# Optimization experiments

Measured on AMD Instinct MI355X. Metric: run time of the kernel, lower is better.

The kernel has to match this reference:

```python
import jax, jax.numpy as jnp
import numpy as np

B, A, T, D, H, NB, OUT = 64, 128, 6, 256, 512, 5, 401
ALPHA = 0.5
BETA = 0.5


def _lin_init(key, n_in, n_out, extra=()):
    bound = 1.0 / np.sqrt(n_in)
    kw, kb = jax.random.split(key)
    W = jax.random.uniform(kw, extra + (n_in, n_out), minval=-bound, maxval=bound, dtype=jnp.float32)
    b = jax.random.uniform(kb, extra + (n_out,), minval=-bound, maxval=bound, dtype=jnp.float32)
    return W, b


def setup_inputs() -> dict:
    key = jax.random.key(0)
    ks = jax.random.split(key, 8)
    stdv = 1.0 / np.sqrt(D)
    anchor = jax.random.uniform(ks[0], (1, 1, T, D), minval=-stdv, maxval=stdv, dtype=jnp.float32)
    sW1, sb1 = _lin_init(ks[1], D, D, (NB,))
    sW2, sb2 = _lin_init(ks[2], D, D, (NB,))
    cW1, cb1 = _lin_init(ks[3], D, D, (NB,))
    cW2, cb2 = _lin_init(ks[4], D, D, (NB,))
    dW1, db1 = _lin_init(ks[5], D, H)
    dW2, db2 = _lin_init(ks[6], H, OUT)
    final_embedding = jax.random.normal(ks[7], (B, A, D), dtype=jnp.float32)
    return {"final_embedding": final_embedding, "anchor": anchor,
            "sW1": sW1, "sb1": sb1, "sW2": sW2, "sb2": sb2,
            "cW1": cW1, "cb1": cb1, "cW2": cW2, "cb2": cb2,
            "dW1": dW1, "db1": db1, "dW2": dW2, "db2": db2}


def _mlp2(x, W1, b1, W2, b2):
    # 2-layer MLP (Linear -> ReLU -> Linear), applied to last dim
    return jax.nn.relu(x @ W1 + b1) @ W2 + b2


def reference(final_embedding, anchor, sW1, sb1, sW2, sb2, cW1, cb1, cW2, cb2, dW1, db1, dW2, db2):
    b, a = final_embedding.shape[:2]
    # s: [B, A, T, D] repeated anchors; c: [B, A, 1, D] context
    s = jnp.broadcast_to(anchor, (b, a, T, D))
    c = final_embedding[:, :, None, :]
    for i in range(NB):
        s_new = _mlp2(s, sW1[i], sb1[i], sW2[i], sb2[i])
        c_new = _mlp2(c, cW1[i], cb1[i], cW2[i], cb2[i])
        s_new = s_new * c_new                      # gate, broadcasts over T
        agg_c = jnp.max(s_new, axis=-2, keepdims=True)
        s = ALPHA * s + BETA * s_new               # sliding running mean
        c = ALPHA * c + BETA * agg_c
    # decoder MLP on trajectory embeddings s: [B, A, T, D]
    res = jax.nn.relu(s @ dW1 + db1) @ dW2 + db2   # [B, A, T, 401]
    coordinates = res[..., :160].reshape(b, a, T, 80, 2)
    av = res[..., 160:240].reshape(b, a, T, 80, 1)
    bv = res[..., 240:320].reshape(b, a, T, 80, 1)
    cv = res[..., 320:400].reshape(b, a, T, 80, 1)
    probas = res[..., -1]                          # [B, A, T]
    cov = jnp.concatenate([jnp.exp(av) * jnp.cosh(bv), jnp.sinh(bv),
                           jnp.sinh(bv), jnp.exp(-av) * jnp.cosh(bv)], axis=-1) * jnp.exp(cv)
    covariance_matrices = cov.reshape(b, a, T, 80, 2, 2)
    return (probas, coordinates, covariance_matrices)
```

## Files before the change

### kernel.cpp

```cpp
#include <hip/hip_runtime.h>
#include <math.h>


constexpr int Tn  = 6;
constexpr int Dn  = 256;
constexpr int Hn  = 512;
constexpr int NBn = 5;
constexpr int OUTn = 401;
constexpr int BA  = 8192;
constexpr int MR  = 49152;
constexpr float kAlpha = 0.5f;
constexpr float kBeta  = 0.5f;

typedef __bf16 bf16_8 __attribute__((ext_vector_type(8)));
typedef float  f32x4  __attribute__((ext_vector_type(4)));

__device__ __forceinline__ void async_copy16(const __bf16* g, __bf16* l) {
  __builtin_amdgcn_global_load_lds(
      (const __attribute__((address_space(1))) void*)g,
      (__attribute__((address_space(3))) void*)l, 16, 0, 0);
}

template<bool RELU, bool OUT_BF16>
__global__ __launch_bounds__(256) void gemm_mfma(
    const __bf16* __restrict__ A, const __bf16* __restrict__ BT,
    const float* __restrict__ bias, void* __restrict__ Cout,
    int M, int N, int K)
{
  __shared__ __align__(16) char smem[34816];

  const int tid = threadIdx.x;
  const int l   = tid & 63;
  const int w   = tid >> 6;
  const int wm  = w >> 1, wn = w & 1;

  const int GX = gridDim.x;
  const int total = GX * gridDim.y;
  const int L = blockIdx.y * GX + blockIdx.x;
  const int xcd = L & 7, pos = L >> 3;
  const int base = total >> 3, rem = total & 7;
  const int start = xcd * base + (xcd < rem ? xcd : rem);
  const int TL = start + pos;
  const int my = TL / GX;
  const int nx = TL - my * GX;
  const int m0 = my * 128;
  const int n0 = nx * 128;

  const int lrow = l >> 2;
  const int lk   = (l & 3) * 8;
  int ar0 = m0 + w * 32 + lrow;        if (ar0 > M - 1) ar0 = M - 1;
  int ar1 = m0 + w * 32 + 16 + lrow;   if (ar1 > M - 1) ar1 = M - 1;
  int br0 = n0 + w * 32 + lrow;        if (br0 > N - 1) br0 = N - 1;
  int br1 = n0 + w * 32 + 16 + lrow;   if (br1 > N - 1) br1 = N - 1;
  const __bf16* Ag0 = A  + (size_t)ar0 * K + lk;
  const __bf16* Ag1 = A  + (size_t)ar1 * K + lk;
  const __bf16* Bg0 = BT + (size_t)br0 * K + lk;
  const __bf16* Bg1 = BT + (size_t)br1 * K + lk;

  f32x4 acc[4][4];
#pragma unroll
  for (int i = 0; i < 4; ++i)
#pragma unroll
    for (int j = 0; j < 4; ++j) acc[i][j] = (f32x4){0.f, 0.f, 0.f, 0.f};

  auto stage = [&](int buf, int ko) {
    __bf16* As = (__bf16*)(smem + buf * 16384);
    __bf16* Bs = As + 4096;
    async_copy16(Ag0 + ko, As + w * 1024);
    async_copy16(Ag1 + ko, As + w * 1024 + 512);
    async_copy16(Bg0 + ko, Bs + w * 1024);
    async_copy16(Bg1 + ko, Bs + w * 1024 + 512);
  };

  const int kIters = K >> 5;
  stage(0, 0);
  __syncthreads();
  for (int kt = 0; kt < kIters; ++kt) {
    if (kt + 1 < kIters) stage((kt + 1) & 1, (kt + 1) * 32);
    const __bf16* As = (const __bf16*)(smem + (kt & 1) * 16384);
    const __bf16* Bs = As + 4096;
    const __bf16* ap = As + (wm * 64 + (l & 15)) * 32 + (l >> 4) * 8;
    const __bf16* bp = Bs + (wn * 64 + (l & 15)) * 32 + (l >> 4) * 8;

    bf16_8 af[4], bf[4];
#pragma unroll
    for (int i = 0; i < 4; ++i) af[i] = *(const bf16_8*)(ap + i * 16 * 32);
#pragma unroll
    for (int j = 0; j < 4; ++j) bf[j] = *(const bf16_8*)(bp + j * 16 * 32);
#pragma unroll
    for (int i = 0; i < 4; ++i)
#pragma unroll
      for (int j = 0; j < 4; ++j)
        acc[i][j] = __builtin_amdgcn_mfma_f32_16x16x32_bf16(af[i], bf[j], acc[i][j], 0, 0, 0);
    __syncthreads();
  }

  const int colb = n0 + wn * 64 + (l & 15);
  const int rowb = m0 + wm * 64 + (l >> 4) * 4;

  if (OUT_BF16) {
    __bf16* Cs = (__bf16*)smem;
    const int lrb = wm * 64 + (l >> 4) * 4;
    const int lcb = wn * 64 + (l & 15);
#pragma unroll
    for (int j = 0; j < 4; ++j) {
      const float bj = bias[colb + j * 16];
#pragma unroll
      for (int i = 0; i < 4; ++i) {
#pragma unroll
        for (int r = 0; r < 4; ++r) {
          float v = acc[i][j][r] + bj;
          if (RELU) v = fmaxf(v, 0.0f);
          Cs[(lrb + i * 16 + r) * 136 + lcb + j * 16] = (__bf16)v;
        }
      }
    }
    __syncthreads();
    __bf16* Cg = (__bf16*)Cout;
#pragma unroll
    for (int it = 0; it < 8; ++it) {
      const int idx = it * 256 + tid;
      const int row = idx >> 4, c16 = idx & 15;
      const int gr = m0 + row;
      if (gr < M) {
        uint4 v = *(const uint4*)(Cs + row * 136 + c16 * 8);
        *(uint4*)(Cg + (size_t)gr * N + n0 + c16 * 8) = v;
      }
    }
  } else {
#pragma unroll
    for (int j = 0; j < 4; ++j) {
      const int gc = colb + j * 16;
      if (gc >= N) continue;
      const float bj = bias[gc];
#pragma unroll
      for (int i = 0; i < 4; ++i) {
        const int gr0 = rowb + i * 16;
#pragma unroll
        for (int r = 0; r < 4; ++r) {
          const int gr = gr0 + r;
          if (gr >= M) continue;
          float v = acc[i][j][r] + bj;
          if (RELU) v = fmaxf(v, 0.0f);
          ((float*)Cout)[(size_t)gr * N + gc] = v;
        }
      }
    }
  }
}

__global__ __launch_bounds__(512) void mlp2_c(
    const __bf16* __restrict__ X, const __bf16* __restrict__ W1T,
    const float* __restrict__ b1, const __bf16* __restrict__ W2T,
    const float* __restrict__ b2, __bf16* __restrict__ Out)
{
  __shared__ __align__(16) char smem[53248];
  __bf16* Hb = (__bf16*)(smem + 36864);

  const int tid = threadIdx.x, l = tid & 63, w = tid >> 6;
  const int m0 = blockIdx.x * 32;
  const int q4 = (l >> 4) * 4;

  f32x4 acc[2][2];
#pragma unroll
  for (int i = 0; i < 2; ++i)
#pragma unroll
    for (int j = 0; j < 2; ++j) acc[i][j] = (f32x4){0.f, 0.f, 0.f, 0.f};

  const __bf16* Xg = X + (size_t)(m0 + (tid >> 2)) * Dn + (tid & 3) * 8;

  auto stageA = [&](int buf, int kt) {
    if (tid < 128)
      async_copy16(Xg + kt * 32, (__bf16*)(smem + buf * 2048) + tid * 8);
  };
  auto stageW = [&](const __bf16* WT, int buf, int kt) {
    __bf16* Wstb = (__bf16*)(smem + 4096 + buf * 16384);
#pragma unroll
    for (int r2 = 0; r2 < 2; ++r2) {
      const int ch = tid + r2 * 512, row = ch >> 2, kk = (ch & 3) * 8;
      async_copy16(WT + (size_t)row * Dn + kt * 32 + kk, Wstb + ch * 8);
    }
  };

  stageA(0, 0); stageW(W1T, 0, 0);
  __syncthreads();
  for (int kt = 0; kt < 8; ++kt) {
    if (kt < 7) { stageA((kt + 1) & 1, kt + 1); stageW(W1T, (kt + 1) & 1, kt + 1); }
    const __bf16* Astb = (const __bf16*)(smem + (kt & 1) * 2048);
    const __bf16* Wstb = (const __bf16*)(smem + 4096 + (kt & 1) * 16384);
    bf16_8 bf[2];
#pragma unroll
    for (int j = 0; j < 2; ++j)
      bf[j] = *(const bf16_8*)(Wstb + (w * 32 + j * 16 + (l & 15)) * 32 + (l >> 4) * 8);
#pragma unroll
    for (int i = 0; i < 2; ++i) {
      bf16_8 af = *(const bf16_8*)(Astb + (i * 16 + (l & 15)) * 32 + (l >> 4) * 8);
#pragma unroll
      for (int j = 0; j < 2; ++j)
        acc[i][j] = __builtin_amdgcn_mfma_f32_16x16x32_bf16(af, bf[j], acc[i][j], 0, 0, 0);
    }
    __syncthreads();
  }

#pragma unroll
  for (int j = 0; j < 2; ++j) {
    const int col = w * 32 + j * 16 + (l & 15);
    const float bj = b1[col];
    __bf16* hc = Hb + (col >> 5) * 1024 + (col & 31);
#pragma unroll
    for (int i = 0; i < 2; ++i)
#pragma unroll
      for (int r = 0; r < 4; ++r) {
        const int row = i * 16 + q4 + r;
        hc[row * 32] = (__bf16)fmaxf(acc[i][j][r] + bj, 0.0f);
      }
  }
  __syncthreads();

#pragma unroll
  for (int i = 0; i < 2; ++i)
#pragma unroll
    for (int j = 0; j < 2; ++j) acc[i][j] = (f32x4){0.f, 0.f, 0.f, 0.f};
  stageW(W2T, 0, 0);
  __syncthreads();
  for (int kt = 0; kt < 8; ++kt) {
    if (kt < 7) stageW(W2T, (kt + 1) & 1, kt + 1);
    const __bf16* Wstb = (const __bf16*)(smem + 4096 + (kt & 1) * 16384);
    bf16_8 bf[2];
#pragma unroll
    for (int j = 0; j < 2; ++j)
      bf[j] = *(const bf16_8*)(Wstb + (w * 32 + j * 16 + (l & 15)) * 32 + (l >> 4) * 8);
#pragma unroll
    for (int i = 0; i < 2; ++i) {
      bf16_8 af = *(const bf16_8*)(Hb + kt * 1024 + (i * 16 + (l & 15)) * 32 + (l >> 4) * 8);
#pragma unroll
      for (int j = 0; j < 2; ++j)
        acc[i][j] = __builtin_amdgcn_mfma_f32_16x16x32_bf16(af, bf[j], acc[i][j], 0, 0, 0);
    }
    __syncthreads();
  }

#pragma unroll
  for (int j = 0; j < 2; ++j) {
    const int col = w * 32 + j * 16 + (l & 15);
    const float bj = b2[col];
#pragma unroll
    for (int i = 0; i < 2; ++i)
#pragma unroll
      for (int r = 0; r < 4; ++r) {
        const int row = i * 16 + q4 + r;
        Out[(size_t)(m0 + row) * Dn + col] = (__bf16)(acc[i][j][r] + bj);
      }
  }
}

__global__ __launch_bounds__(512) void mlp2_cs(
    __bf16* __restrict__ S,
    const __bf16* __restrict__ sW1T, const float* __restrict__ sb1,
    const __bf16* __restrict__ sW2T, const float* __restrict__ sb2,
    const __bf16* __restrict__ cW1T, const float* __restrict__ cb1,
    const __bf16* __restrict__ cW2T, const float* __restrict__ cb2,
    __bf16* __restrict__ C)
{
  __shared__ __align__(16) char smem[71680];
  __bf16* Hb    = (__bf16*)(smem + 22528);
  __bf16* Snew  = (__bf16*)smem;
  __bf16* Hc    = (__bf16*)(smem + 45056);
  __bf16* CnewL = (__bf16*)(smem + 53248);

  const int tid = threadIdx.x, l = tid & 63, w = tid >> 6;
  const int m0  = blockIdx.x * 96;
  const int ba0 = blockIdx.x * 16;
  const int q4  = (l >> 4) * 4;

  {
    f32x4 ac[2];
    ac[0] = (f32x4){0.f, 0.f, 0.f, 0.f};
    ac[1] = (f32x4){0.f, 0.f, 0.f, 0.f};

    const __bf16* Cg = C + (size_t)(ba0 + (tid >> 2)) * Dn + (tid & 3) * 8;

    auto stageC1 = [&](int buf, int kt) {
      __bf16* Astb = (__bf16*)(smem + buf * 22528);
      __bf16* Wstb = Astb + 3072;
      if (tid < 64) async_copy16(Cg + kt * 32, Astb + tid * 8);
#pragma unroll
      for (int r2 = 0; r2 < 2; ++r2) {
        const int ch = tid + r2 * 512, row = ch >> 2, kk = (ch & 3) * 8;
        async_copy16(cW1T + (size_t)row * Dn + kt * 32 + kk, Wstb + ch * 8);
      }
    };
    stageC1(0, 0);
    __syncthreads();
    for (int kt = 0; kt < 8; ++kt) {
      if (kt < 7) stageC1((kt + 1) & 1, kt + 1);
      const __bf16* Astb = (const __bf16*)(smem + (kt & 1) * 22528);
      const __bf16* Wstb = Astb + 3072;
      bf16_8 bf[2];
#pragma unroll
      for (int j = 0; j < 2; ++j)
        bf[j] = *(const bf16_8*)(Wstb + (w * 32 + j * 16 + (l & 15)) * 32 + (l >> 4) * 8);
      bf16_8 af = *(const bf16_8*)(Astb + (l & 15) * 32 + (l >> 4) * 8);
#pragma unroll
      for (int j = 0; j < 2; ++j)
        ac[j] = __builtin_amdgcn_mfma_f32_16x16x32_bf16(af, bf[j], ac[j], 0, 0, 0);
      __syncthreads();
    }

#pragma unroll
    for (int j = 0; j < 2; ++j) {
      const int col = w * 32 + j * 16 + (l & 15);
      const float bj = cb1[col];
      __bf16* hc = Hc + (col >> 5) * 512 + (col & 31);
#pragma unroll
      for (int r = 0; r < 4; ++r)
        hc[(q4 + r) * 32] = (__bf16)fmaxf(ac[j][r] + bj, 0.0f);
    }
    __syncthreads();

    ac[0] = (f32x4){0.f, 0.f, 0.f, 0.f};
    ac[1] = (f32x4){0.f, 0.f, 0.f, 0.f};
    auto stageC2 = [&](int buf, int kt) {
      __bf16* Wstb = (__bf16*)(smem + buf * 22528 + 6144);
#pragma unroll
      for (int r2 = 0; r2 < 2; ++r2) {
        const int ch = tid + r2 * 512, row = ch >> 2, kk = (ch & 3) * 8;
        async_copy16(cW2T + (size_t)row * Dn + kt * 32 + kk, Wstb + ch * 8);
      }
    };
    stageC2(0, 0);
    __syncthreads();
    for (int kt = 0; kt < 8; ++kt) {
      if (kt < 7) stageC2((kt + 1) & 1, kt + 1);
      const __bf16* Wstb = (const __bf16*)(smem + (kt & 1) * 22528 + 6144);
      bf16_8 bf[2];
#pragma unroll
      for (int j = 0; j < 2; ++j)
        bf[j] = *(const bf16_8*)(Wstb + (w * 32 + j * 16 + (l & 15)) * 32 + (l >> 4) * 8);
      bf16_8 af = *(const bf16_8*)(Hc + kt * 512 + (l & 15) * 32 + (l >> 4) * 8);
#pragma unroll
      for (int j = 0; j < 2; ++j)
        ac[j] = __builtin_amdgcn_mfma_f32_16x16x32_bf16(af, bf[j], ac[j], 0, 0, 0);
      __syncthreads();
    }

#pragma unroll
    for (int j = 0; j < 2; ++j) {
      const int col = w * 32 + j * 16 + (l & 15);
      const float bj = cb2[col];
#pragma unroll
      for (int r = 0; r < 4; ++r)
        CnewL[(q4 + r) * 264 + col] = (__bf16)(ac[j][r] + bj);
    }
    __syncthreads();
  }

  bf16_8 cn8 = *(const bf16_8*)(CnewL + (tid >> 5) * 264 + (tid & 31) * 8);

  f32x4 acc[6][2];
#pragma unroll
  for (int i = 0; i < 6; ++i)
#pragma unroll
    for (int j = 0; j < 2; ++j) acc[i][j] = (f32x4){0.f, 0.f, 0.f, 0.f};

  const __bf16* Sg = S + (size_t)(m0 + (tid >> 2)) * Dn + (tid & 3) * 8;

  auto stageL1 = [&](int buf, int kt) {
    __bf16* Astb = (__bf16*)(smem + buf * 22528);
    __bf16* Wstb = (__bf16*)(smem + buf * 22528 + 6144);
    if (tid < 384) async_copy16(Sg + kt * 32, Astb + tid * 8);
#pragma unroll
    for (int r2 = 0; r2 < 2; ++r2) {
      const int ch = tid + r2 * 512, row = ch >> 2, kk = (ch & 3) * 8;
      async_copy16(sW1T + (size_t)row * Dn + kt * 32 + kk, Wstb + ch * 8);
    }
  };

  stageL1(0, 0);
  __syncthreads();
  for (int kt = 0; kt < 8; ++kt) {
    if (kt < 7) stageL1((kt + 1) & 1, kt + 1);
    const __bf16* Astb = (const __bf16*)(smem + (kt & 1) * 22528);
    const __bf16* Wstb = Astb + 3072;
    bf16_8 bf[2];
#pragma unroll
    for (int j = 0; j < 2; ++j)
      bf[j] = *(const bf16_8*)(Wstb + (w * 32 + j * 16 + (l & 15)) * 32 + (l >> 4) * 8);
#pragma unroll
    for (int i = 0; i < 6; ++i) {
      bf16_8 af = *(const bf16_8*)(Astb + (i * 16 + (l & 15)) * 32 + (l >> 4) * 8);
#pragma unroll
      for (int j = 0; j < 2; ++j)
        acc[i][j] = __builtin_amdgcn_mfma_f32_16x16x32_bf16(af, bf[j], acc[i][j], 0, 0, 0);
    }
    __syncthreads();
  }

#pragma unroll
  for (int j = 0; j < 2; ++j) {
    const int col = w * 32 + j * 16 + (l & 15);
    const float bj = sb1[col];
    __bf16* hc = Hb + (col >> 5) * (96 * 32) + (col & 31);
#pragma unroll
    for (int i = 0; i < 6; ++i)
#pragma unroll
      for (int r = 0; r < 4; ++r) {
        const int row = i * 16 + q4 + r;
        hc[row * 32] = (__bf16)fmaxf(acc[i][j][r] + bj, 0.0f);
      }
  }
  __syncthreads();

#pragma unroll
  for (int i = 0; i < 6; ++i)
#pragma unroll
    for (int j = 0; j < 2; ++j) acc[i][j] = (f32x4){0.f, 0.f, 0.f, 0.f};
  __bf16* Wst = (__bf16*)(smem + 6144);
  for (int kt = 0; kt < 8; ++kt) {
#pragma unroll
    for (int r2 = 0; r2 < 2; ++r2) {
      const int ch = tid + r2 * 512, row = ch >> 2, kk = (ch & 3) * 8;
      async_copy16(sW2T + (size_t)row * Dn + kt * 32 + kk, Wst + ch * 8);
    }
    __syncthreads();
    bf16_8 bf[2];
#pragma unroll
    for (int j = 0; j < 2; ++j)
      bf[j] = *(const bf16_8*)(Wst + (w * 32 + j * 16 + (l & 15)) * 32 + (l >> 4) * 8);
#pragma unroll
    for (int i = 0; i < 6; ++i) {
      bf16_8 af = *(const bf16_8*)(Hb + kt * (96 * 32) + (i * 16 + (l & 15)) * 32 + (l >> 4) * 8);
#pragma unroll
      for (int j = 0; j < 2; ++j)
        acc[i][j] = __builtin_amdgcn_mfma_f32_16x16x32_bf16(af, bf[j], acc[i][j], 0, 0, 0);
    }
    __syncthreads();
  }

#pragma unroll
  for (int j = 0; j < 2; ++j) {
    const int col = w * 32 + j * 16 + (l & 15);
    const float bj = sb2[col];
#pragma unroll
    for (int i = 0; i < 6; ++i)
#pragma unroll
      for (int r = 0; r < 4; ++r) {
        const int row = i * 16 + q4 + r;
        Snew[row * 264 + col] = (__bf16)(acc[i][j][r] + bj);
      }
  }
  __syncthreads();

  {
    const int ba = tid >> 5, dg = (tid & 31) * 8;
    const size_t gb = (size_t)(ba0 + ba) * Dn + dg;
    float cn[8], m[8];
#pragma unroll
    for (int e = 0; e < 8; ++e) { cn[e] = (float)cn8[e]; m[e] = -3.402823466e38f; }
#pragma unroll
    for (int t = 0; t < Tn; ++t) {
      const int row = ba * 6 + t;
      bf16_8 sn8 = *(const bf16_8*)(Snew + row * 264 + dg);
      const size_t gs = (size_t)(m0 + row) * Dn + dg;
      bf16_8 s8 = *(const bf16_8*)(S + gs);
      bf16_8 o8;
#pragma unroll
      for (int e = 0; e < 8; ++e) {
        const float sn = (float)sn8[e] * cn[e];
        m[e] = fmaxf(m[e], sn);
        o8[e] = (__bf16)(kAlpha * (float)s8[e] + kBeta * sn);
      }
      *(bf16_8*)(S + gs) = o8;
    }
    bf16_8 c8 = *(const bf16_8*)(C + gb);
#pragma unroll
    for (int e = 0; e < 8; ++e)
      c8[e] = (__bf16)(kAlpha * (float)c8[e] + kBeta * m[e]);
    *(bf16_8*)(C + gb) = c8;
  }
}

__global__ __launch_bounds__(512, 4) void decoder_fused(
    const __bf16* __restrict__ S, const __bf16* __restrict__ W1T,
    const float* __restrict__ b1, const __bf16* __restrict__ W2T,
    const float* __restrict__ bias, float* __restrict__ out)
{
  __shared__ __align__(16) char smem[73728];
  __bf16* Ast = (__bf16*)smem;
  __bf16* W1s = (__bf16*)(smem + 32768);
  __bf16* Hb  = (__bf16*)(smem + 65536);
  float*  mid = (float*)smem;
  float*  coordL = (float*)(smem + 32768);

  const int tid = threadIdx.x, l = tid & 63, w = tid >> 6;
  const int m0 = blockIdx.x * 64;
  const int q4 = (l >> 4) * 4;
  const int rt  = w >> 1;
  const int ch2 = (w & 1) * 32;

  f32x4 acc[4][4];
#pragma unroll
  for (int i = 0; i < 4; ++i)
#pragma unroll
    for (int j = 0; j < 4; ++j) acc[i][j] = (f32x4){0.f, 0.f, 0.f, 0.f};

#pragma unroll
  for (int r4 = 0; r4 < 4; ++r4) {
    const int q = tid + r4 * 512;
    const int ktq = q >> 8, row = (q >> 2) & 63, kk = (q & 3) * 8;
    async_copy16(S + (size_t)(m0 + row) * Dn + ktq * 32 + kk, Ast + q * 8);
  }

  auto stageW1 = [&](int cc) {
#pragma unroll
    for (int r4 = 0; r4 < 4; ++r4) {
      const int q = tid + r4 * 512;
      const int ktq = q >> 8, row = (q >> 2) & 63, kk = (q & 3) * 8;
      async_copy16(W1T + (size_t)(cc * 64 + row) * Dn + ktq * 32 + kk, W1s + q * 8);
    }
  };

  const __bf16* W2p[4];
#pragma unroll
  for (int j = 0; j < 4; ++j) {
    int col = w * 64 + j * 16 + (l & 15);
    if (col > 400) col = 400;
    W2p[j] = W2T + (size_t)col * Hn + (l >> 4) * 8;
  }

  stageW1(0);
  __syncthreads();

  for (int cc = 0; cc < 8; ++cc) {
    f32x4 a1[2];
    a1[0] = (f32x4){0.f, 0.f, 0.f, 0.f};
    a1[1] = (f32x4){0.f, 0.f, 0.f, 0.f};
#pragma unroll
    for (int kt = 0; kt < 8; ++kt) {
      bf16_8 af = *(const bf16_8*)(Ast + kt * 2048 + (rt * 16 + (l & 15)) * 32 + (l >> 4) * 8);
#pragma unroll
      for (int j = 0; j < 2; ++j) {
        bf16_8 bw = *(const bf16_8*)(W1s + kt * 2048 + (ch2 + j * 16 + (l & 15)) * 32 + (l >> 4) * 8);
        a1[j] = __builtin_amdgcn_mfma_f32_16x16x32_bf16(af, bw, a1[j], 0, 0, 0);
      }
    }

#pragma unroll
    for (int j = 0; j < 2; ++j) {
      const int col = ch2 + j * 16 + (l & 15);
      const float bj = b1[cc * 64 + col];
      __bf16* hp = Hb + (col >> 5) * 2048 + (col & 31);
#pragma unroll
      for (int r = 0; r < 4; ++r)
        hp[(rt * 16 + q4 + r) * 32] = (__bf16)fmaxf(a1[j][r] + bj, 0.0f);
    }
    __syncthreads();

    if (cc < 7) stageW1(cc + 1);

#pragma unroll
    for (int kt2 = 0; kt2 < 2; ++kt2) {
      bf16_8 af2[4], bf2[4];
#pragma unroll
      for (int j = 0; j < 4; ++j)
        bf2[j] = *(const bf16_8*)(W2p[j] + cc * 64 + kt2 * 32);
#pragma unroll
      for (int i = 0; i < 4; ++i)
        af2[i] = *(const bf16_8*)(Hb + kt2 * 2048 + (i * 16 + (l & 15)) * 32 + (l >> 4) * 8);
#pragma unroll
      for (int i = 0; i < 4; ++i)
#pragma unroll
        for (int j = 0; j < 4; ++j)
          acc[i][j] = __builtin_amdgcn_mfma_f32_16x16x32_bf16(af2[i], bf2[j], acc[i][j], 0, 0, 0);
    }
    __syncthreads();
  }

  float* cov    = out + MR + (size_t)MR * 160;
  float* coordG = out + MR;
  const int gc = w * 64 + (l & 15);
#pragma unroll
  for (int sub = 0; sub < 2; ++sub) {
#pragma unroll
    for (int ih = 0; ih < 2; ++ih) {
      const int i = sub * 2 + ih;
#pragma unroll
      for (int j = 0; j < 4; ++j) {
        const int c = gc + j * 16;
        if (c > 400) continue;
        const float bj = bias[c];
#pragma unroll
        for (int r = 0; r < 4; ++r) {
          const int lr = ih * 16 + q4 + r;
          const int gr = m0 + sub * 32 + lr;
          const float v = acc[i][j][r] + bj;
          if (c < 160)      coordL[lr * 160 + c] = v;
          else if (c < 400) mid[lr * 241 + (c - 160)] = v;
          else              out[gr] = v;
        }
      }
    }
    __syncthreads();
#pragma unroll
    for (int p = 0; p < 3; ++p) {
      const int q = p * 512 + tid;
      if (q < 1280) {
        const int r32 = q / 40, c4 = q - r32 * 40;
        const int gr = m0 + sub * 32 + r32;
        *(f32x4*)(coordG + (size_t)gr * 160 + c4 * 4) =
            *(const f32x4*)(coordL + r32 * 160 + c4 * 4);
      }
    }
#pragma unroll
    for (int p = 0; p < 5; ++p) {
      const int q = p * 512 + tid;
      const int r32 = q / 80, j = q - r32 * 80;
      const int gr = m0 + sub * 32 + r32;
      const float av = mid[r32 * 241 + j];
      const float bv = mid[r32 * 241 + 80 + j];
      const float cv = mid[r32 * 241 + 160 + j];
      const float eb = __expf(bv), ebn = __expf(-bv);
      const float sh = 0.5f * (eb - ebn), ch = 0.5f * (eb + ebn);
      const float ea = __expf(av), ean = __expf(-av), ec = __expf(cv);
      f32x4 c4 = { ea * ch * ec, sh * ec, sh * ec, ean * ch * ec };
      *(f32x4*)(cov + (size_t)gr * 320 + 4 * j) = c4;
    }
    if (sub == 0) __syncthreads();
  }
}

__global__ __launch_bounds__(256) void transpose_bf16(
    const float* __restrict__ W, __bf16* __restrict__ WT, int K, int N)
{
  __shared__ float t[32][33];
  const int b  = blockIdx.z;
  const int tx = threadIdx.x, ty = threadIdx.y;
  const int k0 = blockIdx.y * 32, n0 = blockIdx.x * 32;
  const float* Wb  = W  + (size_t)b * K * N;
  __bf16*      WTb = WT + (size_t)b * N * K;
#pragma unroll
  for (int r = 0; r < 4; ++r) {
    int kk = k0 + ty + r * 8;
    if (kk < K && n0 + tx < N) t[ty + r * 8][tx] = Wb[(size_t)kk * N + n0 + tx];
  }
  __syncthreads();
#pragma unroll
  for (int r = 0; r < 4; ++r) {
    int nn = n0 + ty + r * 8;
    if (nn < N && k0 + tx < K)
      WTb[(size_t)nn * K + k0 + tx] = (__bf16)t[tx][ty + r * 8];
  }
}

__global__ __launch_bounds__(256) void convert_bf16(
    const float* __restrict__ in, __bf16* __restrict__ out, int n)
{
  int i = blockIdx.x * 256 + threadIdx.x;
  if (i < n) out[i] = (__bf16)in[i];
}

__global__ __launch_bounds__(256) void ew_update0(
    const float* __restrict__ anchor, const float* __restrict__ fe,
    const float* __restrict__ snewsm, const __bf16* __restrict__ cnew,
    __bf16* __restrict__ s, __bf16* __restrict__ c)
{
  int q = blockIdx.x * 256 + threadIdx.x;
  if (q >= BA * 32) return;
  int ba = q >> 5;
  int dg = (q & 31) * 8;
  bf16_8 cn8 = *(const bf16_8*)(cnew + (size_t)ba * Dn + dg);
  float cn[8], m[8];
#pragma unroll
  for (int e = 0; e < 8; ++e) { cn[e] = (float)cn8[e]; m[e] = -3.402823466e38f; }
  size_t base = (size_t)ba * Tn * Dn + dg;
#pragma unroll
  for (int t = 0; t < Tn; ++t) {
    bf16_8 o8;
#pragma unroll
    for (int e = 0; e < 8; ++e) {
      float sn = snewsm[t * Dn + dg + e] * cn[e];
      m[e] = fmaxf(m[e], sn);
      o8[e] = (__bf16)(kAlpha * anchor[t * Dn + dg + e] + kBeta * sn);
    }
    *(bf16_8*)(s + base + t * Dn) = o8;
  }
  bf16_8 c8;
#pragma unroll
  for (int e = 0; e < 8; ++e)
    c8[e] = (__bf16)(kAlpha * fe[(size_t)ba * Dn + dg + e] + kBeta * m[e]);
  *(bf16_8*)(c + (size_t)ba * Dn + dg) = c8;
}

extern "C" void kernel_launch(void* const* d_in, const int* in_sizes, int n_in,
                              void* d_out, int out_size, void* d_ws, size_t ws_size,
                              hipStream_t stream) {
  const float* fe     = (const float*)d_in[0];
  const float* anchor = (const float*)d_in[1];
  const float* sW1 = (const float*)d_in[2];
  const float* sb1 = (const float*)d_in[3];
  const float* sW2 = (const float*)d_in[4];
  const float* sb2 = (const float*)d_in[5];
  const float* cW1 = (const float*)d_in[6];
  const float* cb1 = (const float*)d_in[7];
  const float* cW2 = (const float*)d_in[8];
  const float* cb2 = (const float*)d_in[9];
  const float* dW1 = (const float*)d_in[10];
  const float* db1 = (const float*)d_in[11];
  const float* dW2 = (const float*)d_in[12];
  const float* db2 = (const float*)d_in[13];
  float* out = (float*)d_out;

  char* p = (char*)d_ws;
  __bf16* s_bf    = (__bf16*)(p + 0);
  __bf16* c_bf    = (__bf16*)(p + 75497472);
  __bf16* cnew_bf = (__bf16*)(p + 79691776);
  __bf16* fe_bf   = (__bf16*)(p + 83886080);
  __bf16* sWT1    = (__bf16*)(p + 88080384);
  __bf16* sWT2    = (__bf16*)(p + 88735744);
  __bf16* cWT1    = (__bf16*)(p + 89391104);
  __bf16* cWT2    = (__bf16*)(p + 90046464);
  __bf16* dWT1    = (__bf16*)(p + 90701824);
  __bf16* dWT2    = (__bf16*)(p + 90963968);
  __bf16* anc_bf  = (__bf16*)(p + 91374592);
  __bf16* hsm_bf  = (__bf16*)(p + 91377664);
  float*  snewsm_f= (float* )(p + 91380736);

  auto gemm = [&](const __bf16* A, const __bf16* BT, const float* b, void* C,
                  int M, int N, int K, bool relu, bool outbf) {
    dim3 grid((N + 127) / 128, (M + 127) / 128);
    if (relu) {
      if (outbf) gemm_mfma<true,  true ><<<grid, 256, 0, stream>>>(A, BT, b, C, M, N, K);
      else       gemm_mfma<true,  false><<<grid, 256, 0, stream>>>(A, BT, b, C, M, N, K);
    } else {
      if (outbf) gemm_mfma<false, true ><<<grid, 256, 0, stream>>>(A, BT, b, C, M, N, K);
      else       gemm_mfma<false, false><<<grid, 256, 0, stream>>>(A, BT, b, C, M, N, K);
    }
  };

  {
    dim3 blk(32, 8);
    dim3 g88(8, 8, NBn);
    transpose_bf16<<<g88, blk, 0, stream>>>(sW1, sWT1, Dn, Dn);
    transpose_bf16<<<g88, blk, 0, stream>>>(sW2, sWT2, Dn, Dn);
    transpose_bf16<<<g88, blk, 0, stream>>>(cW1, cWT1, Dn, Dn);
    transpose_bf16<<<g88, blk, 0, stream>>>(cW2, cWT2, Dn, Dn);
    transpose_bf16<<<dim3(16, 8, 1), blk, 0, stream>>>(dW1, dWT1, Dn, Hn);
    transpose_bf16<<<dim3(13, 16, 1), blk, 0, stream>>>(dW2, dWT2, Hn, OUTn);
  }
  convert_bf16<<<(BA * Dn + 255) / 256, 256, 0, stream>>>(fe, fe_bf, BA * Dn);
  convert_bf16<<<(Tn * Dn + 255) / 256, 256, 0, stream>>>(anchor, anc_bf, Tn * Dn);

  const size_t WKK = (size_t)Dn * Dn;

  gemm(anc_bf, sWT1, sb1, hsm_bf,   Tn, Dn, Dn, true,  true);
  gemm(hsm_bf, sWT2, sb2, snewsm_f, Tn, Dn, Dn, false, false);
  mlp2_c<<<BA / 32, 512, 0, stream>>>(fe_bf, cWT1, cb1, cWT2, cb2, cnew_bf);
  ew_update0<<<(BA * 32 + 255) / 256, 256, 0, stream>>>(anchor, fe, snewsm_f,
                                                        cnew_bf, s_bf, c_bf);

  for (int i = 1; i < NBn; ++i) {
    mlp2_cs<<<MR / 96, 512, 0, stream>>>(
        s_bf,
        sWT1 + i * WKK, sb1 + i * Dn, sWT2 + i * WKK, sb2 + i * Dn,
        cWT1 + i * WKK, cb1 + i * Dn, cWT2 + i * WKK, cb2 + i * Dn,
        c_bf);
  }

  decoder_fused<<<MR / 64, 512, 0, stream>>>(s_bf, dWT1, db1, dWT2, db2, out);
}
```

Baseline: 377.6 us.

## Load weight fragments directly from global memory instead of staging through LDS

```diff
diff --git a/kernel.cpp b/kernel.cpp
--- a/kernel.cpp
+++ b/kernel.cpp
@@ -154,52 +154,50 @@
     const float* __restrict__ b1, const __bf16* __restrict__ W2T,
     const float* __restrict__ b2, __bf16* __restrict__ Out)
 {
-  __shared__ __align__(16) char smem[53248];
-  __bf16* Hb = (__bf16*)(smem + 36864);
+  __shared__ __align__(16) char smem[32768];
+  __bf16* Ast = (__bf16*)smem;
+  __bf16* Hb  = (__bf16*)(smem + 16384);
 
   const int tid = threadIdx.x, l = tid & 63, w = tid >> 6;
   const int m0 = blockIdx.x * 32;
   const int q4 = (l >> 4) * 4;
 
+#pragma unroll
+  for (int r2 = 0; r2 < 2; ++r2) {
+    const int q = tid + r2 * 512;
+    const int kt = q >> 7, row = (q >> 2) & 31, kq = q & 3;
+    async_copy16(X + (size_t)(m0 + row) * Dn + kt * 32 + kq * 8, Ast + q * 8);
+  }
+
+  const __bf16* W1p[2];
+  const __bf16* W2p[2];
+#pragma unroll
+  for (int j = 0; j < 2; ++j) {
+    const int col = w * 32 + j * 16 + (l & 15);
+    W1p[j] = W1T + (size_t)col * Dn + (l >> 4) * 8;
+    W2p[j] = W2T + (size_t)col * Dn + (l >> 4) * 8;
+  }
+
   f32x4 acc[2][2];
 #pragma unroll
   for (int i = 0; i < 2; ++i)
 #pragma unroll
     for (int j = 0; j < 2; ++j) acc[i][j] = (f32x4){0.f, 0.f, 0.f, 0.f};
 
-  const __bf16* Xg = X + (size_t)(m0 + (tid >> 2)) * Dn + (tid & 3) * 8;
-
-  auto stageA = [&](int buf, int kt) {
-    if (tid < 128)
-      async_copy16(Xg + kt * 32, (__bf16*)(smem + buf * 2048) + tid * 8);
-  };
-  auto stageW = [&](const __bf16* WT, int buf, int kt) {
-    __bf16* Wstb = (__bf16*)(smem + 4096 + buf * 16384);
-#pragma unroll
-    for (int r2 = 0; r2 < 2; ++r2) {
-      const int ch = tid + r2 * 512, row = ch >> 2, kk = (ch & 3) * 8;
-      async_copy16(WT + (size_t)row * Dn + kt * 32 + kk, Wstb + ch * 8);
-    }
-  };
-
-  stageA(0, 0); stageW(W1T, 0, 0);
-  __syncthreads();
+  __syncthreads();
+
+#pragma unroll
   for (int kt = 0; kt < 8; ++kt) {
-    if (kt < 7) { stageA((kt + 1) & 1, kt + 1); stageW(W1T, (kt + 1) & 1, kt + 1); }
-    const __bf16* Astb = (const __bf16*)(smem + (kt & 1) * 2048);
-    const __bf16* Wstb = (const __bf16*)(smem + 4096 + (kt & 1) * 16384);
     bf16_8 bf[2];
 #pragma unroll
-    for (int j = 0; j < 2; ++j)
-      bf[j] = *(const bf16_8*)(Wstb + (w * 32 + j * 16 + (l & 15)) * 32 + (l >> 4) * 8);
+    for (int j = 0; j < 2; ++j) bf[j] = *(const bf16_8*)(W1p[j] + kt * 32);
 #pragma unroll
     for (int i = 0; i < 2; ++i) {
-      bf16_8 af = *(const bf16_8*)(Astb + (i * 16 + (l & 15)) * 32 + (l >> 4) * 8);
+      bf16_8 af = *(const bf16_8*)(Ast + kt * 1024 + (i * 16 + (l & 15)) * 32 + (l >> 4) * 8);
 #pragma unroll
       for (int j = 0; j < 2; ++j)
         acc[i][j] = __builtin_amdgcn_mfma_f32_16x16x32_bf16(af, bf[j], acc[i][j], 0, 0, 0);
     }
-    __syncthreads();
   }
 
 #pragma unroll
@@ -221,15 +219,11 @@
   for (int i = 0; i < 2; ++i)
 #pragma unroll
     for (int j = 0; j < 2; ++j) acc[i][j] = (f32x4){0.f, 0.f, 0.f, 0.f};
-  stageW(W2T, 0, 0);
-  __syncthreads();
+#pragma unroll
   for (int kt = 0; kt < 8; ++kt) {
-    if (kt < 7) stageW(W2T, (kt + 1) & 1, kt + 1);
-    const __bf16* Wstb = (const __bf16*)(smem + 4096 + (kt & 1) * 16384);
     bf16_8 bf[2];
 #pragma unroll
-    for (int j = 0; j < 2; ++j)
-      bf[j] = *(const bf16_8*)(Wstb + (w * 32 + j * 16 + (l & 15)) * 32 + (l >> 4) * 8);
+    for (int j = 0; j < 2; ++j) bf[j] = *(const bf16_8*)(W2p[j] + kt * 32);
 #pragma unroll
     for (int i = 0; i < 2; ++i) {
       bf16_8 af = *(const bf16_8*)(Hb + kt * 1024 + (i * 16 + (l & 15)) * 32 + (l >> 4) * 8);
@@ -237,7 +231,6 @@
       for (int j = 0; j < 2; ++j)
         acc[i][j] = __builtin_amdgcn_mfma_f32_16x16x32_bf16(af, bf[j], acc[i][j], 0, 0, 0);
     }
-    __syncthreads();
   }
 
 #pragma unroll
@@ -265,6 +258,7 @@
   __shared__ __align__(16) char smem[71680];
   __bf16* Hb    = (__bf16*)(smem + 22528);
   __bf16* Snew  = (__bf16*)smem;
+  __bf16* AstC  = (__bf16*)smem;
   __bf16* Hc    = (__bf16*)(smem + 45056);
   __bf16* CnewL = (__bf16*)(smem + 53248);
 
@@ -273,38 +267,34 @@
   const int ba0 = blockIdx.x * 16;
   const int q4  = (l >> 4) * 4;
 
+  const int fcol = w * 32 + (l & 15);
+  const int foff = (l >> 4) * 8;
+  const __bf16* cW1p0 = cW1T + (size_t)fcol * Dn + foff;
+  const __bf16* cW1p1 = cW1p0 + (size_t)16 * Dn;
+  const __bf16* cW2p0 = cW2T + (size_t)fcol * Dn + foff;
+  const __bf16* cW2p1 = cW2p0 + (size_t)16 * Dn;
+  const __bf16* sW1p0 = sW1T + (size_t)fcol * Dn + foff;
+  const __bf16* sW1p1 = sW1p0 + (size_t)16 * Dn;
+  const __bf16* sW2p0 = sW2T + (size_t)fcol * Dn + foff;
+  const __bf16* sW2p1 = sW2p0 + (size_t)16 * Dn;
+
   {
+    {
+      const int kt = tid >> 6, row = (tid >> 2) & 15, kq = tid & 3;
+      async_copy16(C + (size_t)(ba0 + row) * Dn + kt * 32 + kq * 8, AstC + tid * 8);
+    }
+    __syncthreads();
+
     f32x4 ac[2];
     ac[0] = (f32x4){0.f, 0.f, 0.f, 0.f};
     ac[1] = (f32x4){0.f, 0.f, 0.f, 0.f};
-
-    const __bf16* Cg = C + (size_t)(ba0 + (tid >> 2)) * Dn + (tid & 3) * 8;
-
-    auto stageC1 = [&](int buf, int kt) {
-      __bf16* Astb = (__bf16*)(smem + buf * 22528);
-      __bf16* Wstb = Astb + 3072;
-      if (tid < 64) async_copy16(Cg + kt * 32, Astb + tid * 8);
-#pragma unroll
-      for (int r2 = 0; r2 < 2; ++r2) {
-        const int ch = tid + r2 * 512, row = ch >> 2, kk = (ch & 3) * 8;
-        async_copy16(cW1T + (size_t)row * Dn + kt * 32 + kk, Wstb + ch * 8);
-      }
-    };
-    stageC1(0, 0);
-    __syncthreads();
+#pragma unroll
     for (int kt = 0; kt < 8; ++kt) {
-      if (kt < 7) stageC1((kt + 1) & 1, kt + 1);
-      const __bf16* Astb = (const __bf16*)(smem + (kt & 1) * 22528);
-      const __bf16* Wstb = Astb + 3072;
-      bf16_8 bf[2];
-#pragma unroll
-      for (int j = 0; j < 2; ++j)
-        bf[j] = *(const bf16_8*)(Wstb + (w * 32 + j * 16 + (l & 15)) * 32 + (l >> 4) * 8);
-      bf16_8 af = *(const bf16_8*)(Astb + (l & 15) * 32 + (l >> 4) * 8);
-#pragma unroll
-      for (int j = 0; j < 2; ++j)
-        ac[j] = __builtin_amdgcn_mfma_f32_16x16x32_bf16(af, bf[j], ac[j], 0, 0, 0);
-      __syncthreads();
+      bf16_8 bf0 = *(const bf16_8*)(cW1p0 + kt * 32);
+      bf16_8 bf1 = *(const bf16_8*)(cW1p1 + kt * 32);
+      bf16_8 af = *(const bf16_8*)(AstC + kt * 512 + (l & 15) * 32 + (l >> 4) * 8);
+      ac[0] = __builtin_amdgcn_mfma_f32_16x16x32_bf16(af, bf0, ac[0], 0, 0, 0);
+      ac[1] = __builtin_amdgcn_mfma_f32_16x16x32_bf16(af, bf1, ac[1], 0, 0, 0);
     }
 
 #pragma unroll
@@ -320,28 +310,13 @@
 
     ac[0] = (f32x4){0.f, 0.f, 0.f, 0.f};
     ac[1] = (f32x4){0.f, 0.f, 0.f, 0.f};
-    auto stageC2 = [&](int buf, int kt) {
-      __bf16* Wstb = (__bf16*)(smem + buf * 22528 + 6144);
-#pragma unroll
-      for (int r2 = 0; r2 < 2; ++r2) {
-        const int ch = tid + r2 * 512, row = ch >> 2, kk = (ch & 3) * 8;
-        async_copy16(cW2T + (size_t)row * Dn + kt * 32 + kk, Wstb + ch * 8);
-      }
-    };
-    stageC2(0, 0);
-    __syncthreads();
+#pragma unroll
     for (int kt = 0; kt < 8; ++kt) {
-      if (kt < 7) stageC2((kt + 1) & 1, kt + 1);
-      const __bf16* Wstb = (const __bf16*)(smem + (kt & 1) * 22528 + 6144);
-      bf16_8 bf[2];
-#pragma unroll
-      for (int j = 0; j < 2; ++j)
-        bf[j] = *(const bf16_8*)(Wstb + (w * 32 + j * 16 + (l & 15)) * 32 + (l >> 4) * 8);
+      bf16_8 bf0 = *(const bf16_8*)(cW2p0 + kt * 32);
+      bf16_8 bf1 = *(const bf16_8*)(cW2p1 + kt * 32);
       bf16_8 af = *(const bf16_8*)(Hc + kt * 512 + (l & 15) * 32 + (l >> 4) * 8);
-#pragma unroll
-      for (int j = 0; j < 2; ++j)
-        ac[j] = __builtin_amdgcn_mfma_f32_16x16x32_bf16(af, bf[j], ac[j], 0, 0, 0);
-      __syncthreads();
+      ac[0] = __builtin_amdgcn_mfma_f32_16x16x32_bf16(af, bf0, ac[0], 0, 0, 0);
+      ac[1] = __builtin_amdgcn_mfma_f32_16x16x32_bf16(af, bf1, ac[1], 0, 0, 0);
     }
 
 #pragma unroll
@@ -350,7 +325,7 @@
       const float bj = cb2[col];
 #pragma unroll
       for (int r = 0; r < 4; ++r)
-        CnewL[(q4 + r) * 264 + col] = (__bf16)(ac[j][r] + bj);
+        CnewL[(q4 + r) * 264 + col] = (__bf16)((j ? ac[1][r] : ac[0][r]) + bj);
     }
     __syncthreads();
   }
@@ -365,33 +340,23 @@
 
   const __bf16* Sg = S + (size_t)(m0 + (tid >> 2)) * Dn + (tid & 3) * 8;
 
-  auto stageL1 = [&](int buf, int kt) {
-    __bf16* Astb = (__bf16*)(smem + buf * 22528);
-    __bf16* Wstb = (__bf16*)(smem + buf * 22528 + 6144);
-    if (tid < 384) async_copy16(Sg + kt * 32, Astb + tid * 8);
-#pragma unroll
-    for (int r2 = 0; r2 < 2; ++r2) {
-      const int ch = tid + r2 * 512, row = ch >> 2, kk = (ch & 3) * 8;
-      async_copy16(sW1T + (size_t)row * Dn + kt * 32 + kk, Wstb + ch * 8);
-    }
+  auto stageA = [&](int buf, int kt) {
+    if (tid < 384)
+      async_copy16(Sg + kt * 32, (__bf16*)(smem + buf * 6144) + tid * 8);
   };
 
-  stageL1(0, 0);
+  stageA(0, 0);
   __syncthreads();
   for (int kt = 0; kt < 8; ++kt) {
-    if (kt < 7) stageL1((kt + 1) & 1, kt + 1);
-    const __bf16* Astb = (const __bf16*)(smem + (kt & 1) * 22528);
-    const __bf16* Wstb = Astb + 3072;
-    bf16_8 bf[2];
-#pragma unroll
-    for (int j = 0; j < 2; ++j)
-      bf[j] = *(const bf16_8*)(Wstb + (w * 32 + j * 16 + (l & 15)) * 32 + (l >> 4) * 8);
+    if (kt < 7) stageA((kt + 1) & 1, kt + 1);
+    const __bf16* Astb = (const __bf16*)(smem + (kt & 1) * 6144);
+    bf16_8 bf0 = *(const bf16_8*)(sW1p0 + kt * 32);
+    bf16_8 bf1 = *(const bf16_8*)(sW1p1 + kt * 32);
 #pragma unroll
     for (int i = 0; i < 6; ++i) {
       bf16_8 af = *(const bf16_8*)(Astb + (i * 16 + (l & 15)) * 32 + (l >> 4) * 8);
-#pragma unroll
-      for (int j = 0; j < 2; ++j)
-        acc[i][j] = __builtin_amdgcn_mfma_f32_16x16x32_bf16(af, bf[j], acc[i][j], 0, 0, 0);
+      acc[i][0] = __builtin_amdgcn_mfma_f32_16x16x32_bf16(af, bf0, acc[i][0], 0, 0, 0);
+      acc[i][1] = __builtin_amdgcn_mfma_f32_16x16x32_bf16(af, bf1, acc[i][1], 0, 0, 0);
     }
     __syncthreads();
   }
@@ -415,27 +380,18 @@
   for (int i = 0; i < 6; ++i)
 #pragma unroll
     for (int j = 0; j < 2; ++j) acc[i][j] = (f32x4){0.f, 0.f, 0.f, 0.f};
-  __bf16* Wst = (__bf16*)(smem + 6144);
+#pragma unroll
   for (int kt = 0; kt < 8; ++kt) {
-#pragma unroll
-    for (int r2 = 0; r2 < 2; ++r2) {
-      const int ch = tid + r2 * 512, row = ch >> 2, kk = (ch & 3) * 8;
-      async_copy16(sW2T + (size_t)row * Dn + kt * 32 + kk, Wst + ch * 8);
-    }
-    __syncthreads();
-    bf16_8 bf[2];
-#pragma unroll
-    for (int j = 0; j < 2; ++j)
-      bf[j] = *(const bf16_8*)(Wst + (w * 32 + j * 16 + (l & 15)) * 32 + (l >> 4) * 8);
+    bf16_8 bf0 = *(const bf16_8*)(sW2p0 + kt * 32);
+    bf16_8 bf1 = *(const bf16_8*)(sW2p1 + kt * 32);
 #pragma unroll
     for (int i = 0; i < 6; ++i) {
       bf16_8 af = *(const bf16_8*)(Hb + kt * (96 * 32) + (i * 16 + (l & 15)) * 32 + (l >> 4) * 8);
-#pragma unroll
-      for (int j = 0; j < 2; ++j)
-        acc[i][j] = __builtin_amdgcn_mfma_f32_16x16x32_bf16(af, bf[j], acc[i][j], 0, 0, 0);
-    }
-    __syncthreads();
-  }
+      acc[i][0] = __builtin_amdgcn_mfma_f32_16x16x32_bf16(af, bf0, acc[i][0], 0, 0, 0);
+      acc[i][1] = __builtin_amdgcn_mfma_f32_16x16x32_bf16(af, bf1, acc[i][1], 0, 0, 0);
+    }
+  }
+  __syncthreads();
 
 #pragma unroll
   for (int j = 0; j < 2; ++j) {
@@ -485,10 +441,9 @@
     const float* __restrict__ b1, const __bf16* __restrict__ W2T,
     const float* __restrict__ bias, float* __restrict__ out)
 {
-  __shared__ __align__(16) char smem[73728];
+  __shared__ __align__(16) char smem[53248];
   __bf16* Ast = (__bf16*)smem;
-  __bf16* W1s = (__bf16*)(smem + 32768);
-  __bf16* Hb  = (__bf16*)(smem + 65536);
+  __bf16* Hb  = (__bf16*)(smem + 32768);
   float*  mid = (float*)smem;
   float*  coordL = (float*)(smem + 32768);
 
@@ -511,14 +466,10 @@
     async_copy16(S + (size_t)(m0 + row) * Dn + ktq * 32 + kk, Ast + q * 8);
   }
 
-  auto stageW1 = [&](int cc) {
-#pragma unroll
-    for (int r4 = 0; r4 < 4; ++r4) {
-      const int q = tid + r4 * 512;
-      const int ktq = q >> 8, row = (q >> 2) & 63, kk = (q & 3) * 8;
-      async_copy16(W1T + (size_t)(cc * 64 + row) * Dn + ktq * 32 + kk, W1s + q * 8);
-    }
-  };
+  const __bf16* W1p[2];
+#pragma unroll
+  for (int j = 0; j < 2; ++j)
+    W1p[j] = W1T + (size_t)(ch2 + j * 16 + (l & 15)) * Dn + (l >> 4) * 8;
 
   const __bf16* W2p[4];
 #pragma unroll
@@ -528,7 +479,6 @@
     W2p[j] = W2T + (size_t)col * Hn + (l >> 4) * 8;
   }
 
-  stageW1(0);
   __syncthreads();
 
   for (int cc = 0; cc < 8; ++cc) {
@@ -537,12 +487,11 @@
     a1[1] = (f32x4){0.f, 0.f, 0.f, 0.f};
 #pragma unroll
     for (int kt = 0; kt < 8; ++kt) {
+      bf16_8 bw0 = *(const bf16_8*)(W1p[0] + (size_t)cc * 64 * Dn + kt * 32);
+      bf16_8 bw1 = *(const bf16_8*)(W1p[1] + (size_t)cc * 64 * Dn + kt * 32);
       bf16_8 af = *(const bf16_8*)(Ast + kt * 2048 + (rt * 16 + (l & 15)) * 32 + (l >> 4) * 8);
-#pragma unroll
-      for (int j = 0; j < 2; ++j) {
-        bf16_8 bw = *(const bf16_8*)(W1s + kt * 2048 + (ch2 + j * 16 + (l & 15)) * 32 + (l >> 4) * 8);
-        a1[j] = __builtin_amdgcn_mfma_f32_16x16x32_bf16(af, bw, a1[j], 0, 0, 0);
-      }
+      a1[0] = __builtin_amdgcn_mfma_f32_16x16x32_bf16(af, bw0, a1[0], 0, 0, 0);
+      a1[1] = __builtin_amdgcn_mfma_f32_16x16x32_bf16(af, bw1, a1[1], 0, 0, 0);
     }
 
 #pragma unroll
@@ -555,8 +504,6 @@
         hp[(rt * 16 + q4 + r) * 32] = (__bf16)fmaxf(a1[j][r] + bj, 0.0f);
     }
     __syncthreads();
-
-    if (cc < 7) stageW1(cc + 1);
 
 #pragma unroll
     for (int kt2 = 0; kt2 < 2; ++kt2) {
```

Measured after the change: 478.5 us. 1.27x slower.
